# Optimization experiments

Measured on AMD Instinct MI355X. Metric: run time of the kernel, lower is better.

The kernel has to match this reference:

```python
import jax, jax.numpy as jnp
import numpy as np
from jax import lax

NUM_SAMPLE_POINTS = 1024
BIG = jnp.float32(1e10)  # stands in for +inf, fp16-safe


def setup_inputs() -> dict:
    key = jax.random.key(0)
    input = jax.random.normal(key, (8, 65536, 3), dtype=jnp.float32)
    return {"input": input}


def _fps_indices(points, num_samples):
    # points: [B, N, 3] -> indices [B, num_samples] int32
    B, N, _ = points.shape

    def step(carry, _):
        min_dist, farthest = carry  # [B, N], [B]
        cur = jnp.take_along_axis(points, farthest[:, None, None], axis=1)  # [B,1,3]
        d = jnp.sum((points - cur) ** 2, axis=-1)  # [B, N] squared distances
        min_dist = jnp.minimum(min_dist, d)
        nxt = jnp.argmax(min_dist, axis=-1).astype(jnp.int32)  # [B]
        return (min_dist, nxt), farthest

    init = (jnp.full((B, N), BIG, dtype=points.dtype), jnp.zeros((B,), jnp.int32))
    _, idx = lax.scan(step, init, None, length=num_samples)  # idx: [M, B]
    return idx.T  # [B, M]


def reference(input):
    # Faithful FPS: iteratively pick the point farthest from the selected set,
    # starting from index 0 (standard PointNet++ convention).
    idx = _fps_indices(input, NUM_SAMPLE_POINTS)  # [B, M] int32
    sampled = jnp.take_along_axis(input, idx[:, :, None], axis=1)  # [B, M, 3]
    return idx, sampled
```

## Files before the change

### kernel.cpp

```cpp
#include <hip/hip_runtime.h>


#define NB    8
#define NPTS  65536
#define NSAMP 1024
#define WPB   32
#define TPB   512
#define NWAVE 8
#define PPT   4
#define RECQ  16

typedef unsigned long long ull;

#define DPP(x, ctrl) \
  ((unsigned)__builtin_amdgcn_update_dpp((int)(x), (int)(x), (ctrl), 0xf, 0xf, false))

__device__ __forceinline__ unsigned umax_wave64(unsigned x) {
  unsigned t;
  t = DPP(x, 0x111); x = t > x ? t : x;
  t = DPP(x, 0x112); x = t > x ? t : x;
  t = DPP(x, 0x114); x = t > x ? t : x;
  t = DPP(x, 0x118); x = t > x ? t : x;
  t = DPP(x, 0x142); x = t > x ? t : x;
  t = DPP(x, 0x143); x = t > x ? t : x;
  return (unsigned)__builtin_amdgcn_readlane((int)x, 63);
}
__device__ __forceinline__ unsigned umax_low8(unsigned x) {
  unsigned t;
  t = DPP(x, 0x111); x = t > x ? t : x;
  t = DPP(x, 0x112); x = t > x ? t : x;
  t = DPP(x, 0x114); x = t > x ? t : x;
  return (unsigned)__builtin_amdgcn_readlane((int)x, 7);
}

__device__ __forceinline__ void ld3_issue(const ull* p, ull& a, ull& b, ull& c) {
  asm volatile(
      "global_load_dwordx2 %0, %3, off sc0\n\t"
      "global_load_dwordx2 %1, %3, off offset:8 sc0\n\t"
      "global_load_dwordx2 %2, %3, off offset:16 sc0"
      : "=&v"(a), "=&v"(b), "=&v"(c) : "v"(p) : "memory");
}
__device__ __forceinline__ void wait3_touch(ull& a, ull& b, ull& c) {
  asm volatile("s_waitcnt vmcnt(3)" : "+v"(a), "+v"(b), "+v"(c) :: "memory");
}
__device__ __forceinline__ void wait_vm0() {
  asm volatile("s_waitcnt vmcnt(0)" ::: "memory");
}
__device__ __forceinline__ void st3_sc0(ull* p, ull a, ull b, ull c) {
  asm volatile(
      "global_store_dwordx2 %3, %0, off sc0\n\t"
      "global_store_dwordx2 %3, %1, off offset:8 sc0\n\t"
      "global_store_dwordx2 %3, %2, off offset:16 sc0"
      :: "v"(a), "v"(b), "v"(c), "v"(p) : "memory");
}

__device__ __forceinline__ void stage2_pack(const unsigned (*red)[5], int lane,
                                            ull tag, ull& w0, ull& w1, ull& w2,
                                            int& ewin) {
  const int e = lane & 7;
  const unsigned d2 = red[e][0];
  const unsigned nn = red[e][1];
  const unsigned mx = umax_low8(d2);
  const ull bb = __ballot(d2 == mx) & 0xFFull;
  if (__popcll(bb) == 1) {
    ewin = __ffsll(bb) - 1;
  } else {
    const unsigned v = (d2 == mx) ? (65535u - nn) : 0u;
    const unsigned mv = umax_low8(v);
    const ull b2 = __ballot((d2 == mx) && (v == mv)) & 0xFFull;
    ewin = __ffsll(b2) - 1;
  }
  const ull k2 = ((ull)d2 << 16) | (ull)(65535u - nn);
  const unsigned xb = red[e][2], yb = red[e][3], zb = red[e][4];
  w0 = (k2 << 16) | tag;
  w1 = ((ull)xb << 32) | ((ull)(yb >> 16) << 16) | tag;
  w2 = ((ull)(yb & 0xFFFFu) << 48) | ((ull)zb << 16) | tag;
}

__global__ __launch_bounds__(TPB, 4)
void fps_kernel(const float* __restrict__ pts, float* __restrict__ out,
                ull* __restrict__ ws) {
  const int wg   = blockIdx.x;
  const int b    = wg >> 5;
  const int w    = wg & 31;
  const int tid  = threadIdx.x;
  const int lane = tid & 63;
  const int wave = tid >> 6;

  const float* p = pts + (size_t)b * NPTS * 3;

  float px[PPT], py[PPT], pz[PPT], md[PPT];
#pragma unroll
  for (int i = 0; i < PPT; ++i) {
    const int n = w * (TPB * PPT) + i * TPB + tid;
    px[i] = p[3 * n + 0];
    py[i] = p[3 * n + 1];
    pz[i] = p[3 * n + 2];
    md[i] = 1e10f;
  }

  float cx = p[0], cy = p[1], cz = p[2];

  ull* baseL = ws + (size_t)b * (2 * WPB * RECQ);
  ull* baseI = ws + (size_t)NB * (2 * WPB * RECQ) + (size_t)b * (2 * WPB * RECQ);

  float* out_idx = out + (size_t)b * NSAMP;
  float* out_smp = out + (size_t)NB * NSAMP + (size_t)b * NSAMP * 3;

  if (w == 0 && tid == 0) {
    out_idx[0] = 0.0f;
    out_smp[0] = cx; out_smp[1] = cy; out_smp[2] = cz;
  }

  __shared__ unsigned red[NWAVE][5];
  __shared__ float4 bc4;
  __shared__ int bn2;

  bool useIF = false;

  for (int t = 0; t < NSAMP - 1; ++t) {
    float bv = -1.0f; int bi = 0;
#pragma unroll
    for (int i = 0; i < PPT; ++i) {
      const float dx = __fsub_rn(px[i], cx);
      const float dy = __fsub_rn(py[i], cy);
      const float dz = __fsub_rn(pz[i], cz);
      const float d  = __fadd_rn(__fadd_rn(__fmul_rn(dx, dx), __fmul_rn(dy, dy)),
                                 __fmul_rn(dz, dz));
      const float m = fminf(md[i], d);
      md[i] = m;
      if (m > bv) { bv = m; bi = i; }
    }

    const unsigned dbits = __float_as_uint(bv);
    const unsigned mw = umax_wave64(dbits);
    const bool tied = (dbits == mw);
    const ull bal0 = __ballot(tied);
    int wlane;
    if (__popcll(bal0) == 1) {
      wlane = __ffsll(bal0) - 1;
    } else {
      ull sel = 0;
#pragma unroll
      for (int ii = 0; ii < PPT; ++ii) {
        const ull bb = __ballot(tied && (bi == ii));
        const bool take = (sel == 0) && (bb != 0);
        sel = take ? bb : sel;
      }
      wlane = __ffsll(sel) - 1;
    }
    if (lane == wlane) {
      const bool c1 = (bi & 1), c2 = (bi & 2);
      const float qx = c2 ? (c1 ? px[3] : px[2]) : (c1 ? px[1] : px[0]);
      const float qy = c2 ? (c1 ? py[3] : py[2]) : (c1 ? py[1] : py[0]);
      const float qz = c2 ? (c1 ? pz[3] : pz[2]) : (c1 ? pz[1] : pz[0]);
      red[wave][0] = dbits;
      red[wave][1] = (unsigned)(w * (TPB * PPT) + bi * TPB + tid);
      red[wave][2] = __float_as_uint(qx);
      red[wave][3] = __float_as_uint(qy);
      red[wave][4] = __float_as_uint(qz);
    }
    __syncthreads();

    const ull tag = (ull)(unsigned)(t + 1);
    const int par = t & 1;

    if (wave == 1) {
      ull w0, w1, w2; int ewin;
      stage2_pack(red, lane, tag, w0, w1, w2, ewin);
      if (lane == ewin) {
        st3_sc0(baseL + (size_t)(par * WPB + w) * RECQ, w0, w1, w2);
        ull* recI = baseI + (size_t)(par * WPB + w) * RECQ;
        __hip_atomic_store(recI + 0, w0, __ATOMIC_RELAXED, __HIP_MEMORY_SCOPE_AGENT);
        __hip_atomic_store(recI + 1, w1, __ATOMIC_RELAXED, __HIP_MEMORY_SCOPE_AGENT);
        __hip_atomic_store(recI + 2, w2, __ATOMIC_RELAXED, __HIP_MEMORY_SCOPE_AGENT);
      }
    } else if (wave == 0) {
      const size_t roff = (size_t)(par * WPB + (lane & 31)) * RECQ;
      const ull* recL = baseL + roff;
      const ull* recI = baseI + roff;
      const bool mine = (lane < WPB);
      ull r0 = 0, r1 = 0, r2 = 0;
      bool s = !mine;

      if (!useIF) {
        if (mine) {
          ull a0, a1, a2, b0, b1, b2;
          bool fromA = true, hit = false;
          ld3_issue(recL, a0, a1, a2);
          for (int it = 0; it < 128; ++it) {
            ld3_issue(recL, b0, b1, b2);
            wait3_touch(a0, a1, a2);
            bool m = ((a0 & 0xFFFFull) == tag) & ((a1 & 0xFFFFull) == tag) &
                     ((a2 & 0xFFFFull) == tag);
            if (__all(m)) { hit = true; fromA = true; break; }
            ld3_issue(recL, a0, a1, a2);
            wait3_touch(b0, b1, b2);
            m = ((b0 & 0xFFFFull) == tag) & ((b1 & 0xFFFFull) == tag) &
                ((b2 & 0xFFFFull) == tag);
            if (__all(m)) { hit = true; fromA = false; break; }
          }
          wait_vm0();
          if (hit) {
            if (fromA) { r0 = a0; r1 = a1; r2 = a2; }
            else       { r0 = b0; r1 = b1; r2 = b2; }
            s = true;
          }
        }
      }

      if (!__all(s)) {
        useIF = true;
        bool done = !mine;
        for (;;) {
          if (!done) {
            r0 = __hip_atomic_load(recI + 0, __ATOMIC_RELAXED, __HIP_MEMORY_SCOPE_AGENT);
            r1 = __hip_atomic_load(recI + 1, __ATOMIC_RELAXED, __HIP_MEMORY_SCOPE_AGENT);
            r2 = __hip_atomic_load(recI + 2, __ATOMIC_RELAXED, __HIP_MEMORY_SCOPE_AGENT);
            done = ((r0 & 0xFFFFull) == tag) & ((r1 & 0xFFFFull) == tag) &
                   ((r2 & 0xFFFFull) == tag);
          }
          if (__all(done)) break;
          __builtin_amdgcn_s_sleep(1);
        }
      }

      const unsigned d3  = (unsigned)(r0 >> 32);
      const unsigned lnv = (unsigned)((r0 >> 16) & 0xFFFFull);
      const unsigned m3 = umax_wave64(d3);
      const ull b3 = __ballot(d3 == m3);
      int src;
      if (__popcll(b3) == 1) {
        src = __ffsll(b3) - 1;
      } else {
        const unsigned v = (d3 == m3) ? lnv : 0u;
        const unsigned mv = umax_wave64(v);
        const ull b4 = __ballot((d3 == m3) && (v == mv));
        src = __ffsll(b4) - 1;
      }
      const float xx = __uint_as_float((unsigned)(r1 >> 32));
      const float yy = __uint_as_float(((unsigned)((r1 >> 16) & 0xFFFFull) << 16) |
                                       (unsigned)(r2 >> 48));
      const float zz = __uint_as_float((unsigned)((r2 >> 16) & 0xFFFFFFFFull));
      const int n2   = 65535 - (int)__shfl((int)lnv, src, 64);
      const float wx = __shfl(xx, src, 64);
      const float wy = __shfl(yy, src, 64);
      const float wz = __shfl(zz, src, 64);
      if (lane == 0) {
        bc4 = make_float4(wx, wy, wz, 0.0f);
        bn2 = n2;
      }
    }
    __syncthreads();

    const float4 c4 = bc4;
    if (w == 0 && wave == 2 && lane == 0) {
      out_idx[t + 1] = (float)bn2;
      out_smp[(t + 1) * 3 + 0] = c4.x;
      out_smp[(t + 1) * 3 + 1] = c4.y;
      out_smp[(t + 1) * 3 + 2] = c4.z;
    }
    cx = c4.x; cy = c4.y; cz = c4.z;
  }
}

extern "C" void kernel_launch(void* const* d_in, const int* in_sizes, int n_in,
                              void* d_out, int out_size, void* d_ws, size_t ws_size,
                              hipStream_t stream) {
  (void)in_sizes; (void)n_in; (void)out_size; (void)ws_size;
  const float* pts = (const float*)d_in[0];
  float* out = (float*)d_out;
  ull* ws = (ull*)d_ws;
  fps_kernel<<<dim3(NB * WPB), dim3(TPB), 0, stream>>>(pts, out, ws);
}
```

Baseline: 2.140 ms.

## Have every wave poll cross-block records directly and drop the LDS broadcast barrier

Each wave now polls the per-block candidate records in global memory and runs the final wave-level argmax itself. This removes the second __syncthreads and the LDS hop through which wave 0 broadcast the chosen point each iteration. The record layout also changes from one 128-byte slot per block to a structure-of-arrays with a 32-entry stride, so the 32 polling lanes read contiguous words and each load coalesces. The trade-off is eight times more polling traffic per block against the shared flags, which could add memory contention across the cooperating blocks.

```diff
diff --git a/kernel.cpp b/kernel.cpp
--- a/kernel.cpp
+++ b/kernel.cpp
@@ -8,7 +8,7 @@
 #define TPB   512
 #define NWAVE 8
 #define PPT   4
-#define RECQ  16
+#define WSTR  32
 
 typedef unsigned long long ull;
 
@@ -36,8 +36,8 @@
 __device__ __forceinline__ void ld3_issue(const ull* p, ull& a, ull& b, ull& c) {
   asm volatile(
       "global_load_dwordx2 %0, %3, off sc0\n\t"
-      "global_load_dwordx2 %1, %3, off offset:8 sc0\n\t"
-      "global_load_dwordx2 %2, %3, off offset:16 sc0"
+      "global_load_dwordx2 %1, %3, off offset:256 sc0\n\t"
+      "global_load_dwordx2 %2, %3, off offset:512 sc0"
       : "=&v"(a), "=&v"(b), "=&v"(c) : "v"(p) : "memory");
 }
 __device__ __forceinline__ void wait3_touch(ull& a, ull& b, ull& c) {
@@ -49,8 +49,8 @@
 __device__ __forceinline__ void st3_sc0(ull* p, ull a, ull b, ull c) {
   asm volatile(
       "global_store_dwordx2 %3, %0, off sc0\n\t"
-      "global_store_dwordx2 %3, %1, off offset:8 sc0\n\t"
-      "global_store_dwordx2 %3, %2, off offset:16 sc0"
+      "global_store_dwordx2 %3, %1, off offset:256 sc0\n\t"
+      "global_store_dwordx2 %3, %2, off offset:512 sc0"
       :: "v"(a), "v"(b), "v"(c), "v"(p) : "memory");
 }
 
@@ -101,8 +101,8 @@
 
   float cx = p[0], cy = p[1], cz = p[2];
 
-  ull* baseL = ws + (size_t)b * (2 * WPB * RECQ);
-  ull* baseI = ws + (size_t)NB * (2 * WPB * RECQ) + (size_t)b * (2 * WPB * RECQ);
+  ull* baseL = ws + (size_t)b * (2 * 3 * WSTR);
+  ull* baseI = ws + (size_t)NB * (2 * 3 * WSTR) + (size_t)b * (2 * 3 * WSTR);
 
   float* out_idx = out + (size_t)b * NSAMP;
   float* out_smp = out + (size_t)NB * NSAMP + (size_t)b * NSAMP * 3;
@@ -113,8 +113,6 @@
   }
 
   __shared__ unsigned red[NWAVE][5];
-  __shared__ float4 bc4;
-  __shared__ int bn2;
 
   bool useIF = false;
 
@@ -169,98 +167,93 @@
       ull w0, w1, w2; int ewin;
       stage2_pack(red, lane, tag, w0, w1, w2, ewin);
       if (lane == ewin) {
-        st3_sc0(baseL + (size_t)(par * WPB + w) * RECQ, w0, w1, w2);
-        ull* recI = baseI + (size_t)(par * WPB + w) * RECQ;
-        __hip_atomic_store(recI + 0, w0, __ATOMIC_RELAXED, __HIP_MEMORY_SCOPE_AGENT);
-        __hip_atomic_store(recI + 1, w1, __ATOMIC_RELAXED, __HIP_MEMORY_SCOPE_AGENT);
-        __hip_atomic_store(recI + 2, w2, __ATOMIC_RELAXED, __HIP_MEMORY_SCOPE_AGENT);
-      }
-    } else if (wave == 0) {
-      const size_t roff = (size_t)(par * WPB + (lane & 31)) * RECQ;
-      const ull* recL = baseL + roff;
-      const ull* recI = baseI + roff;
-      const bool mine = (lane < WPB);
-      ull r0 = 0, r1 = 0, r2 = 0;
-      bool s = !mine;
-
-      if (!useIF) {
-        if (mine) {
-          ull a0, a1, a2, b0, b1, b2;
-          bool fromA = true, hit = false;
+        ull* slotL = baseL + (size_t)par * (3 * WSTR) + w;
+        st3_sc0(slotL, w0, w1, w2);
+        ull* slotI = baseI + (size_t)par * (3 * WSTR) + w;
+        __hip_atomic_store(slotI,            w0, __ATOMIC_RELAXED, __HIP_MEMORY_SCOPE_AGENT);
+        __hip_atomic_store(slotI + WSTR,     w1, __ATOMIC_RELAXED, __HIP_MEMORY_SCOPE_AGENT);
+        __hip_atomic_store(slotI + 2 * WSTR, w2, __ATOMIC_RELAXED, __HIP_MEMORY_SCOPE_AGENT);
+      }
+    }
+
+    const size_t roff = (size_t)par * (3 * WSTR) + (size_t)(lane & 31);
+    const ull* recL = baseL + roff;
+    const ull* recI = baseI + roff;
+    const bool mine = (lane < WPB);
+    ull r0 = 0, r1 = 0, r2 = 0;
+    bool s = !mine;
+
+    if (!useIF) {
+      if (mine) {
+        ull a0, a1, a2, b0, b1, b2;
+        bool fromA = true, hit = false;
+        ld3_issue(recL, a0, a1, a2);
+        for (int it = 0; it < 128; ++it) {
+          ld3_issue(recL, b0, b1, b2);
+          wait3_touch(a0, a1, a2);
+          bool m = ((a0 & 0xFFFFull) == tag) & ((a1 & 0xFFFFull) == tag) &
+                   ((a2 & 0xFFFFull) == tag);
+          if (__all(m)) { hit = true; fromA = true; break; }
           ld3_issue(recL, a0, a1, a2);
-          for (int it = 0; it < 128; ++it) {
-            ld3_issue(recL, b0, b1, b2);
-            wait3_touch(a0, a1, a2);
-            bool m = ((a0 & 0xFFFFull) == tag) & ((a1 & 0xFFFFull) == tag) &
-                     ((a2 & 0xFFFFull) == tag);
-            if (__all(m)) { hit = true; fromA = true; break; }
-            ld3_issue(recL, a0, a1, a2);
-            wait3_touch(b0, b1, b2);
-            m = ((b0 & 0xFFFFull) == tag) & ((b1 & 0xFFFFull) == tag) &
-                ((b2 & 0xFFFFull) == tag);
-            if (__all(m)) { hit = true; fromA = false; break; }
-          }
-          wait_vm0();
-          if (hit) {
-            if (fromA) { r0 = a0; r1 = a1; r2 = a2; }
-            else       { r0 = b0; r1 = b1; r2 = b2; }
-            s = true;
-          }
+          wait3_touch(b0, b1, b2);
+          m = ((b0 & 0xFFFFull) == tag) & ((b1 & 0xFFFFull) == tag) &
+              ((b2 & 0xFFFFull) == tag);
+          if (__all(m)) { hit = true; fromA = false; break; }
         }
-      }
-
-      if (!__all(s)) {
-        useIF = true;
-        bool done = !mine;
-        for (;;) {
-          if (!done) {
-            r0 = __hip_atomic_load(recI + 0, __ATOMIC_RELAXED, __HIP_MEMORY_SCOPE_AGENT);
-            r1 = __hip_atomic_load(recI + 1, __ATOMIC_RELAXED, __HIP_MEMORY_SCOPE_AGENT);
-            r2 = __hip_atomic_load(recI + 2, __ATOMIC_RELAXED, __HIP_MEMORY_SCOPE_AGENT);
-            done = ((r0 & 0xFFFFull) == tag) & ((r1 & 0xFFFFull) == tag) &
-                   ((r2 & 0xFFFFull) == tag);
-          }
-          if (__all(done)) break;
-          __builtin_amdgcn_s_sleep(1);
+        wait_vm0();
+        if (hit) {
+          if (fromA) { r0 = a0; r1 = a1; r2 = a2; }
+          else       { r0 = b0; r1 = b1; r2 = b2; }
+          s = true;
         }
       }
-
-      const unsigned d3  = (unsigned)(r0 >> 32);
-      const unsigned lnv = (unsigned)((r0 >> 16) & 0xFFFFull);
-      const unsigned m3 = umax_wave64(d3);
-      const ull b3 = __ballot(d3 == m3);
-      int src;
-      if (__popcll(b3) == 1) {
-        src = __ffsll(b3) - 1;
-      } else {
-        const unsigned v = (d3 == m3) ? lnv : 0u;
-        const unsigned mv = umax_wave64(v);
-        const ull b4 = __ballot((d3 == m3) && (v == mv));
-        src = __ffsll(b4) - 1;
-      }
-      const float xx = __uint_as_float((unsigned)(r1 >> 32));
-      const float yy = __uint_as_float(((unsigned)((r1 >> 16) & 0xFFFFull) << 16) |
-                                       (unsigned)(r2 >> 48));
-      const float zz = __uint_as_float((unsigned)((r2 >> 16) & 0xFFFFFFFFull));
-      const int n2   = 65535 - (int)__shfl((int)lnv, src, 64);
-      const float wx = __shfl(xx, src, 64);
-      const float wy = __shfl(yy, src, 64);
-      const float wz = __shfl(zz, src, 64);
-      if (lane == 0) {
-        bc4 = make_float4(wx, wy, wz, 0.0f);
-        bn2 = n2;
-      }
-    }
-    __syncthreads();
-
-    const float4 c4 = bc4;
+    }
+
+    if (!__all(s)) {
+      useIF = true;
+      bool done = !mine;
+      for (;;) {
+        if (!done) {
+          r0 = __hip_atomic_load(recI,            __ATOMIC_RELAXED, __HIP_MEMORY_SCOPE_AGENT);
+          r1 = __hip_atomic_load(recI + WSTR,     __ATOMIC_RELAXED, __HIP_MEMORY_SCOPE_AGENT);
+          r2 = __hip_atomic_load(recI + 2 * WSTR, __ATOMIC_RELAXED, __HIP_MEMORY_SCOPE_AGENT);
+          done = ((r0 & 0xFFFFull) == tag) & ((r1 & 0xFFFFull) == tag) &
+                 ((r2 & 0xFFFFull) == tag);
+        }
+        if (__all(done)) break;
+        __builtin_amdgcn_s_sleep(1);
+      }
+    }
+
+    const unsigned d3  = (unsigned)(r0 >> 32);
+    const unsigned lnv = (unsigned)((r0 >> 16) & 0xFFFFull);
+    const unsigned m3 = umax_wave64(d3);
+    const ull b3 = __ballot(d3 == m3);
+    int src;
+    if (__popcll(b3) == 1) {
+      src = __ffsll(b3) - 1;
+    } else {
+      const unsigned v = (d3 == m3) ? lnv : 0u;
+      const unsigned mv = umax_wave64(v);
+      const ull b4 = __ballot((d3 == m3) && (v == mv));
+      src = __ffsll(b4) - 1;
+    }
+    const float xx = __uint_as_float((unsigned)(r1 >> 32));
+    const float yy = __uint_as_float(((unsigned)((r1 >> 16) & 0xFFFFull) << 16) |
+                                     (unsigned)(r2 >> 48));
+    const float zz = __uint_as_float((unsigned)((r2 >> 16) & 0xFFFFFFFFull));
+    const int n2   = 65535 - (int)__shfl((int)lnv, src, 64);
+    const float wx = __shfl(xx, src, 64);
+    const float wy = __shfl(yy, src, 64);
+    const float wz = __shfl(zz, src, 64);
+
     if (w == 0 && wave == 2 && lane == 0) {
-      out_idx[t + 1] = (float)bn2;
-      out_smp[(t + 1) * 3 + 0] = c4.x;
-      out_smp[(t + 1) * 3 + 1] = c4.y;
-      out_smp[(t + 1) * 3 + 2] = c4.z;
-    }
-    cx = c4.x; cy = c4.y; cz = c4.z;
+      out_idx[t + 1] = (float)n2;
+      out_smp[(t + 1) * 3 + 0] = wx;
+      out_smp[(t + 1) * 3 + 1] = wy;
+      out_smp[(t + 1) * 3 + 2] = wz;
+    }
+    cx = wx; cy = wy; cz = wz;
   }
 }
 
```

Result: slower. 3.565 ms (+66.6%).

## Replace block barrier with last-arriver counter and deepen cross-block polling pipeline

Applied to the files above, without the earlier changes.

Drops the per-iteration __syncthreads before the cross-block reduction. Each wave now bumps a shared counter, and the last wave to arrive packs and publishes the block's partial result, using double-buffered reduction slots. The polling wave also issues its spin loads early, before the distance compute, and keeps four loads in flight instead of two, so the latency of seeing peer blocks' results is hidden. The interface-record stores move to a different lane. Risks include LDS visibility ordering without a barrier, a correct counter reset protocol, and extra memory traffic from speculative loads.

```diff
diff --git a/kernel.cpp b/kernel.cpp
--- a/kernel.cpp
+++ b/kernel.cpp
@@ -40,8 +40,8 @@
       "global_load_dwordx2 %2, %3, off offset:16 sc0"
       : "=&v"(a), "=&v"(b), "=&v"(c) : "v"(p) : "memory");
 }
-__device__ __forceinline__ void wait3_touch(ull& a, ull& b, ull& c) {
-  asm volatile("s_waitcnt vmcnt(3)" : "+v"(a), "+v"(b), "+v"(c) :: "memory");
+__device__ __forceinline__ void wait9_touch(ull& a, ull& b, ull& c) {
+  asm volatile("s_waitcnt vmcnt(9)" : "+v"(a), "+v"(b), "+v"(c) :: "memory");
 }
 __device__ __forceinline__ void wait_vm0() {
   asm volatile("s_waitcnt vmcnt(0)" ::: "memory");
@@ -52,6 +52,11 @@
       "global_store_dwordx2 %3, %1, off offset:8 sc0\n\t"
       "global_store_dwordx2 %3, %2, off offset:16 sc0"
       :: "v"(a), "v"(b), "v"(c), "v"(p) : "memory");
+}
+
+__device__ __forceinline__ bool tag3(ull a, ull b, ull c, ull tag) {
+  return ((a & 0xFFFFull) == tag) & ((b & 0xFFFFull) == tag) &
+         ((c & 0xFFFFull) == tag);
 }
 
 __device__ __forceinline__ void stage2_pack(const unsigned (*red)[5], int lane,
@@ -112,13 +117,31 @@
     out_smp[0] = cx; out_smp[1] = cy; out_smp[2] = cz;
   }
 
-  __shared__ unsigned red[NWAVE][5];
+  __shared__ unsigned red[2][NWAVE][5];
+  __shared__ unsigned cnt[2];
   __shared__ float4 bc4;
   __shared__ int bn2;
 
+  if (tid == 0) { cnt[0] = 0u; cnt[1] = 0u; }
+  __syncthreads();
+
   bool useIF = false;
+  ull A0 = 0, A1 = 0, A2 = 0, B0 = 0, B1 = 0, B2 = 0;
+  ull C0 = 0, C1 = 0, C2 = 0, D0 = 0, D1 = 0, D2 = 0;
 
   for (int t = 0; t < NSAMP - 1; ++t) {
+    const ull tag = (ull)(unsigned)(t + 1);
+    const int par = t & 1;
+    const size_t roff = (size_t)(par * WPB + (lane & 31)) * RECQ;
+
+    if (wave == 0 && !useIF && lane < WPB) {
+      const ull* recL = baseL + roff;
+      ld3_issue(recL, A0, A1, A2);
+      ld3_issue(recL, B0, B1, B2);
+      ld3_issue(recL, C0, C1, C2);
+      ld3_issue(recL, D0, D1, D2);
+    }
+
     float bv = -1.0f; int bi = 0;
 #pragma unroll
     for (int i = 0; i < PPT; ++i) {
@@ -154,56 +177,64 @@
       const float qx = c2 ? (c1 ? px[3] : px[2]) : (c1 ? px[1] : px[0]);
       const float qy = c2 ? (c1 ? py[3] : py[2]) : (c1 ? py[1] : py[0]);
       const float qz = c2 ? (c1 ? pz[3] : pz[2]) : (c1 ? pz[1] : pz[0]);
-      red[wave][0] = dbits;
-      red[wave][1] = (unsigned)(w * (TPB * PPT) + bi * TPB + tid);
-      red[wave][2] = __float_as_uint(qx);
-      red[wave][3] = __float_as_uint(qy);
-      red[wave][4] = __float_as_uint(qz);
-    }
-    __syncthreads();
-
-    const ull tag = (ull)(unsigned)(t + 1);
-    const int par = t & 1;
-
-    if (wave == 1) {
+      red[par][wave][0] = dbits;
+      red[par][wave][1] = (unsigned)(w * (TPB * PPT) + bi * TPB + tid);
+      red[par][wave][2] = __float_as_uint(qx);
+      red[par][wave][3] = __float_as_uint(qy);
+      red[par][wave][4] = __float_as_uint(qz);
+    }
+    asm volatile("s_waitcnt lgkmcnt(0)" ::: "memory");
+
+    unsigned old0 = 0;
+    if (lane == 0) old0 = atomicAdd(&cnt[par], 1u);
+    old0 = (unsigned)__shfl((int)old0, 0, 64);
+
+    if (old0 == 7u) {
       ull w0, w1, w2; int ewin;
-      stage2_pack(red, lane, tag, w0, w1, w2, ewin);
+      stage2_pack(red[par], lane, tag, w0, w1, w2, ewin);
+      const size_t so = (size_t)(par * WPB + w) * RECQ;
       if (lane == ewin) {
-        st3_sc0(baseL + (size_t)(par * WPB + w) * RECQ, w0, w1, w2);
-        ull* recI = baseI + (size_t)(par * WPB + w) * RECQ;
+        st3_sc0(baseL + so, w0, w1, w2);
+      }
+      if (lane == ewin + 8) {
+        ull* recI = baseI + so;
         __hip_atomic_store(recI + 0, w0, __ATOMIC_RELAXED, __HIP_MEMORY_SCOPE_AGENT);
         __hip_atomic_store(recI + 1, w1, __ATOMIC_RELAXED, __HIP_MEMORY_SCOPE_AGENT);
         __hip_atomic_store(recI + 2, w2, __ATOMIC_RELAXED, __HIP_MEMORY_SCOPE_AGENT);
       }
-    } else if (wave == 0) {
-      const size_t roff = (size_t)(par * WPB + (lane & 31)) * RECQ;
+      if (lane == 0) cnt[par ^ 1] = 0u;
+    }
+
+    if (wave == 0) {
+      const bool mine = (lane < WPB);
       const ull* recL = baseL + roff;
       const ull* recI = baseI + roff;
-      const bool mine = (lane < WPB);
       ull r0 = 0, r1 = 0, r2 = 0;
       bool s = !mine;
 
       if (!useIF) {
         if (mine) {
-          ull a0, a1, a2, b0, b1, b2;
-          bool fromA = true, hit = false;
-          ld3_issue(recL, a0, a1, a2);
-          for (int it = 0; it < 128; ++it) {
-            ld3_issue(recL, b0, b1, b2);
-            wait3_touch(a0, a1, a2);
-            bool m = ((a0 & 0xFFFFull) == tag) & ((a1 & 0xFFFFull) == tag) &
-                     ((a2 & 0xFFFFull) == tag);
-            if (__all(m)) { hit = true; fromA = true; break; }
-            ld3_issue(recL, a0, a1, a2);
-            wait3_touch(b0, b1, b2);
-            m = ((b0 & 0xFFFFull) == tag) & ((b1 & 0xFFFFull) == tag) &
-                ((b2 & 0xFFFFull) == tag);
-            if (__all(m)) { hit = true; fromA = false; break; }
+          bool hit = false; int from = 0;
+          for (int it = 0; it < 96; ++it) {
+            wait9_touch(A0, A1, A2);
+            if (__all(tag3(A0, A1, A2, tag))) { hit = true; from = 0; break; }
+            ld3_issue(recL, A0, A1, A2);
+            wait9_touch(B0, B1, B2);
+            if (__all(tag3(B0, B1, B2, tag))) { hit = true; from = 1; break; }
+            ld3_issue(recL, B0, B1, B2);
+            wait9_touch(C0, C1, C2);
+            if (__all(tag3(C0, C1, C2, tag))) { hit = true; from = 2; break; }
+            ld3_issue(recL, C0, C1, C2);
+            wait9_touch(D0, D1, D2);
+            if (__all(tag3(D0, D1, D2, tag))) { hit = true; from = 3; break; }
+            ld3_issue(recL, D0, D1, D2);
           }
           wait_vm0();
           if (hit) {
-            if (fromA) { r0 = a0; r1 = a1; r2 = a2; }
-            else       { r0 = b0; r1 = b1; r2 = b2; }
+            if (from == 0)      { r0 = A0; r1 = A1; r2 = A2; }
+            else if (from == 1) { r0 = B0; r1 = B1; r2 = B2; }
+            else if (from == 2) { r0 = C0; r1 = C1; r2 = C2; }
+            else                { r0 = D0; r1 = D1; r2 = D2; }
             s = true;
           }
         }
@@ -217,8 +248,7 @@
             r0 = __hip_atomic_load(recI + 0, __ATOMIC_RELAXED, __HIP_MEMORY_SCOPE_AGENT);
             r1 = __hip_atomic_load(recI + 1, __ATOMIC_RELAXED, __HIP_MEMORY_SCOPE_AGENT);
             r2 = __hip_atomic_load(recI + 2, __ATOMIC_RELAXED, __HIP_MEMORY_SCOPE_AGENT);
-            done = ((r0 & 0xFFFFull) == tag) & ((r1 & 0xFFFFull) == tag) &
-                   ((r2 & 0xFFFFull) == tag);
+            done = tag3(r0, r1, r2, tag);
           }
           if (__all(done)) break;
           __builtin_amdgcn_s_sleep(1);
```

New measurement: 2.406 ms. 1.12x slower.
